# Optimization experiments

Measured on AMD Instinct MI355X. Metric: run time of the kernel, lower is better.

## Reference

```python
import jax, jax.numpy as jnp
import numpy as np

BN_EPS = 1e-5
SAMPLE_KEY = jax.random.key(42)


def setup_inputs() -> dict:
    key = jax.random.key(0)
    ks = jax.random.split(key, 12)
    B, W, E = 524288, 8, 4
    D = W * E  # 32, input dim of fc1

    def lin(k, fan_in, fan_out):
        k1, k2 = jax.random.split(k)
        bound = 1.0 / np.sqrt(fan_in)
        w = jax.random.uniform(k1, (fan_in, fan_out), jnp.float32, -bound, bound)
        b = jax.random.uniform(k2, (fan_out,), jnp.float32, -bound, bound)
        return w, b

    W1, b1 = lin(ks[0], D, 50)
    W2, b2 = lin(ks[1], 50, 30)
    W3, b3 = lin(ks[2], 30, 20)
    W4, b4 = lin(ks[3], 20, 15)
    W5, b5 = lin(ks[4], 15, W)
    # BatchNorm affine params (eval mode, running_mean=0, running_var=1)
    g1, be1 = jnp.ones((50,), jnp.float32), jnp.zeros((50,), jnp.float32)
    g2, be2 = jnp.ones((30,), jnp.float32), jnp.zeros((30,), jnp.float32)
    g3, be3 = jnp.ones((20,), jnp.float32), jnp.zeros((20,), jnp.float32)
    events = jax.random.normal(ks[5], (B, W, E), jnp.float32)
    return {"events": events,
            "W1": W1, "b1": b1, "g1": g1, "be1": be1,
            "W2": W2, "b2": b2, "g2": g2, "be2": be2,
            "W3": W3, "b3": b3, "g3": g3, "be3": be3,
            "W4": W4, "b4": b4, "W5": W5, "b5": b5}


def _bn_eval(x, g, b):
    # eval-mode BatchNorm1d with running_mean=0, running_var=1
    return x * (g / jnp.sqrt(1.0 + BN_EPS)) + b


def _probs(events, W1, b1, g1, be1, W2, b2, g2, be2, W3, b3, g3, be3, W4, b4, W5, b5):
    B = events.shape[0]
    x = events.reshape(B, -1)  # (B, window*event_size)
    h = jax.nn.relu(_bn_eval(x @ W1 + b1, g1, be1))
    h = jax.nn.relu(_bn_eval(h @ W2 + b2, g2, be2))
    h = jax.nn.relu(_bn_eval(h @ W3 + b3, g3, be3))
    h = jax.nn.relu(h @ W4 + b4)
    return jax.nn.sigmoid(h @ W5 + b5)  # (B, window_size)


def reference(events, W1, b1, g1, be1, W2, b2, g2, be2, W3, b3, g3, be3, W4, b4, W5, b5):
    p = _probs(events, W1, b1, g1, be1, W2, b2, g2, be2, W3, b3, g3, be3, W4, b4, W5, b5)
    # np.random.choice([0,1], p=[p, 1-p]) => P(choice=1) = 1 - p
    choice = jax.random.bernoulli(SAMPLE_KEY, 1.0 - p).astype(p.dtype)  # (B, W)
    chosen_events_np = 1.0 - choice
    flipped = jnp.abs(choice - p)            # prob of sampled outcome per element
    log_prob = jnp.log(jnp.prod(flipped, axis=1))  # (B,)
    return chosen_events_np, log_prob
```

## Files before the change

### kernel.cpp

```cpp
#include <hip/hip_runtime.h>
#include <math.h>

#define THREADS 256
#define TPW 4
#define ROWS_PER_BLOCK 256
#define P_MARGIN 2e-4f
#define FIXCAP 64

typedef float f32x4 __attribute__((ext_vector_type(4)));
typedef short short8 __attribute__((ext_vector_type(8)));
union Frag { unsigned u[4]; short8 s; };

#define FR1 0
#define FR2 2048
#define FR3 4096
#define VB1 5120
#define VS1 5170
#define VE1 5220
#define VB2 5270
#define VS2 5300
#define VE2 5330
#define VB3 5360
#define VS3 5380
#define VE3 5400
#define VB4 5420
#define VB5 5435
#define ACT 5460
#define WPOOL (ACT + 4 * 1088)
#define FRT4 ACT
#define FRT5 (ACT + 512)

__device__ __forceinline__ void tf2x32(unsigned x0, unsigned x1,
                                       unsigned &o0, unsigned &o1) {
  const unsigned k0 = 0u;
  const unsigned k1 = 42u;
  const unsigned k2 = 0x1BD11BDAu ^ k0 ^ k1;
  x0 += k0; x1 += k1;
#define TF_R(r) { x0 += x1; x1 = (x1 << (r)) | (x1 >> (32 - (r))); x1 ^= x0; }
  TF_R(13) TF_R(15) TF_R(26) TF_R(6)
  x0 += k1; x1 += k2 + 1u;
  TF_R(17) TF_R(29) TF_R(16) TF_R(24)
  x0 += k2; x1 += k0 + 2u;
  TF_R(13) TF_R(15) TF_R(26) TF_R(6)
  x0 += k0; x1 += k1 + 3u;
  TF_R(17) TF_R(29) TF_R(16) TF_R(24)
  x0 += k1; x1 += k2 + 4u;
  TF_R(13) TF_R(15) TF_R(26) TF_R(6)
  x0 += k2; x1 += k0 + 5u;
#undef TF_R
  o0 = x0; o1 = x1;
}

__device__ __forceinline__ unsigned rtnb(float v) {
  unsigned b = __float_as_uint(v);
  return (b + 0x7FFFu + ((b >> 16) & 1u)) & 0xFFFF0000u;
}

__device__ __forceinline__ unsigned cvtpk(float a, float b) {
  unsigned r;
  asm("v_cvt_pk_bf16_f32 %0, %1, %2" : "=v"(r) : "v"(a), "v"(b));
  return r;
}

__device__ __forceinline__ void pack8(const float f[8], short8 &H, short8 &L) {
  Frag h, l;
#pragma unroll
  for (int d = 0; d < 4; ++d) {
    unsigned hd = cvtpk(f[2 * d], f[2 * d + 1]);
    h.u[d] = hd;
    float r0 = f[2 * d]     - __uint_as_float(hd << 16);
    float r1 = f[2 * d + 1] - __uint_as_float(hd & 0xFFFF0000u);
    l.u[d] = cvtpk(r0, r1);
  }
  H = h.s; L = l.s;
}

__device__ __forceinline__ f32x4 mfma16(short8 a, short8 b, f32x4 c) {
  return __builtin_amdgcn_mfma_f32_16x16x32_bf16(a, b, c, 0, 0, 0);
}

__device__ __forceinline__ short8 ldfrag(const float *sW, int dwoff) {
  return *reinterpret_cast<const short8 *>(sW + dwoff);
}

template <int K, int N, int NT, int FB>
__device__ __forceinline__ void stage_layer(const float *__restrict__ W,
                                            float *sW, int t) {
  for (int i = t; i < K * N; i += THREADS) {
    int k = i / N, c = i - k * N;
    float v = W[i];
    unsigned hb = rtnb(v);
    float lov = v - __uint_as_float(hb);
    unsigned lb = rtnb(lov);
    int kt = k >> 5, gg = (k >> 3) & 3, d = (k >> 1) & 3, par = k & 1;
    int nt = c >> 4, lane = gg * 16 + (c & 15);
    int combo = kt * NT + nt;
    int dwhi = FB + (combo * 2 + 0) * 256 + lane * 4 + d;
    unsigned short *hp = reinterpret_cast<unsigned short *>(sW);
    hp[2 * dwhi + par] = (unsigned short)(hb >> 16);
    hp[2 * (dwhi + 256) + par] = (unsigned short)(lb >> 16);
  }
}

__device__ __forceinline__ void loadA(const float *actw, int kbase, int c,
                                      int g, short8 &H, short8 &L) {
  float f[8];
#pragma unroll
  for (int e = 0; e < 8; ++e) f[e] = actw[(kbase + g * 8 + e) * 17 + c];
  pack8(f, H, L);
}

__global__ __launch_bounds__(THREADS, 2)
void wtf_kernel(const float* __restrict__ events,
                const float* __restrict__ W1, const float* __restrict__ b1,
                const float* __restrict__ g1, const float* __restrict__ be1,
                const float* __restrict__ W2, const float* __restrict__ b2,
                const float* __restrict__ g2, const float* __restrict__ be2,
                const float* __restrict__ W3, const float* __restrict__ b3,
                const float* __restrict__ g3, const float* __restrict__ be3,
                const float* __restrict__ W4, const float* __restrict__ b4,
                const float* __restrict__ W5, const float* __restrict__ b5,
                float* __restrict__ out_chosen,
                float* __restrict__ out_logp,
                int B) {
  __shared__ float sW[WPOOL];
  __shared__ unsigned s_cnt;
  __shared__ unsigned s_rows[FIXCAP];

  const int t = threadIdx.x;
  const float rden = (float)(1.0 / sqrt(1.0 + 1e-5));

  if (t == 0) s_cnt = 0;
  for (int i = t; i < ACT + 1024; i += THREADS) sW[i] = 0.f;
  __syncthreads();
  stage_layer<32, 50, 4, FR1>(W1, sW, t);
  stage_layer<50, 30, 2, FR2>(W2, sW, t);
  stage_layer<30, 20, 2, FR3>(W3, sW, t);
  stage_layer<20, 15, 1, FRT4>(W4, sW, t);
  stage_layer<15, 8, 1, FRT5>(W5, sW, t);
  if (t < 50)                  { sW[VB1 + t] = b1[t]; sW[VS1 + t] = g1[t] * rden; sW[VE1 + t] = be1[t]; }
  else if (t >= 64 && t < 94)  { int i = t - 64;  sW[VB2 + i] = b2[i]; sW[VS2 + i] = g2[i] * rden; sW[VE2 + i] = be2[i]; }
  else if (t >= 128 && t < 148){ int i = t - 128; sW[VB3 + i] = b3[i]; sW[VS3 + i] = g3[i] * rden; sW[VE3 + i] = be3[i]; }
  else if (t >= 192 && t < 207){ sW[VB4 + (t - 192)] = b4[t - 192]; }
  else if (t >= 224 && t < 232){ sW[VB5 + (t - 224)] = b5[t - 224]; }
  __syncthreads();

  const int w = t >> 6, lane = t & 63;
  const int c = lane & 15, g = lane >> 4;

  const short8 bh4 = ldfrag(sW, FRT4 + lane * 4);
  const short8 bl4 = ldfrag(sW, FRT4 + 256 + lane * 4);
  const short8 bh5 = ldfrag(sW, FRT5 + lane * 4);
  const short8 bl5 = ldfrag(sW, FRT5 + 256 + lane * 4);
  __syncthreads();

  float *actw = sW + ACT + w * 1088;
  float *ptw  = actw + 544;

  const int wrow0 = blockIdx.x * ROWS_PER_BLOCK + w * (TPW * 16);
  const float4 *xp = reinterpret_cast<const float4 *>(
      events + (size_t)(wrow0 + c) * 32 + g * 8);
  float4 xa = xp[0], xb = xp[1];

#pragma unroll 1
  for (int tt = 0; tt < TPW; ++tt) {
    const int r0 = wrow0 + tt * 16;

    float xf[8] = {xa.x, xa.y, xa.z, xa.w, xb.x, xb.y, xb.z, xb.w};
    short8 Xh, Xl; pack8(xf, Xh, Xl);
    const int ttn = (tt + 1 < TPW) ? tt + 1 : tt;
    xa = xp[ttn * 128]; xb = xp[ttn * 128 + 1];

    {
      f32x4 acc[4];
#pragma unroll
      for (int nt = 0; nt < 4; ++nt) {
        float bb = sW[VB1 + nt * 16 + c];
        f32x4 ci = {bb, bb, bb, bb};
        short8 bh = ldfrag(sW, FR1 + (nt * 2 + 0) * 256 + lane * 4);
        short8 bl = ldfrag(sW, FR1 + (nt * 2 + 1) * 256 + lane * 4);
        ci = mfma16(Xl, bh, ci);
        ci = mfma16(Xh, bl, ci);
        acc[nt] = mfma16(Xh, bh, ci);
      }
#pragma unroll
      for (int nt = 0; nt < 4; ++nt) {
        float sc = sW[VS1 + nt * 16 + c], of = sW[VE1 + nt * 16 + c];
#pragma unroll
        for (int r = 0; r < 4; ++r)
          actw[(nt * 16 + c) * 17 + g * 4 + r] =
              fmaxf(fmaf(acc[nt][r], sc, of), 0.f);
      }
    }

    {
      f32x4 acc[2];
#pragma unroll
      for (int nt = 0; nt < 2; ++nt) {
        float bb = sW[VB2 + nt * 16 + c];
        acc[nt] = f32x4{bb, bb, bb, bb};
      }
#pragma unroll
      for (int kt = 0; kt < 2; ++kt) {
        short8 Ah, Al; loadA(actw, kt * 32, c, g, Ah, Al);
#pragma unroll
        for (int nt = 0; nt < 2; ++nt) {
          short8 bh = ldfrag(sW, FR2 + ((kt * 2 + nt) * 2 + 0) * 256 + lane * 4);
          short8 bl = ldfrag(sW, FR2 + ((kt * 2 + nt) * 2 + 1) * 256 + lane * 4);
          acc[nt] = mfma16(Al, bh, acc[nt]);
          acc[nt] = mfma16(Ah, bl, acc[nt]);
          acc[nt] = mfma16(Ah, bh, acc[nt]);
        }
      }
#pragma unroll
      for (int nt = 0; nt < 2; ++nt) {
        float sc = sW[VS2 + nt * 16 + c], of = sW[VE2 + nt * 16 + c];
#pragma unroll
        for (int r = 0; r < 4; ++r)
          actw[(nt * 16 + c) * 17 + g * 4 + r] =
              fmaxf(fmaf(acc[nt][r], sc, of), 0.f);
      }
    }

    {
      f32x4 acc[2];
#pragma unroll
      for (int nt = 0; nt < 2; ++nt) {
        float bb = sW[VB3 + nt * 16 + c];
        acc[nt] = f32x4{bb, bb, bb, bb};
      }
      short8 Ah, Al; loadA(actw, 0, c, g, Ah, Al);
#pragma unroll
      for (int nt = 0; nt < 2; ++nt) {
        short8 bh = ldfrag(sW, FR3 + (nt * 2 + 0) * 256 + lane * 4);
        short8 bl = ldfrag(sW, FR3 + (nt * 2 + 1) * 256 + lane * 4);
        acc[nt] = mfma16(Al, bh, acc[nt]);
        acc[nt] = mfma16(Ah, bl, acc[nt]);
        acc[nt] = mfma16(Ah, bh, acc[nt]);
      }
#pragma unroll
      for (int nt = 0; nt < 2; ++nt) {
        float sc = sW[VS3 + nt * 16 + c], of = sW[VE3 + nt * 16 + c];
#pragma unroll
        for (int r = 0; r < 4; ++r)
          actw[(nt * 16 + c) * 17 + g * 4 + r] =
              fmaxf(fmaf(acc[nt][r], sc, of), 0.f);
      }
    }

    {
      float bb = sW[VB4 + c];
      f32x4 acc = {bb, bb, bb, bb};
      short8 Ah, Al; loadA(actw, 0, c, g, Ah, Al);
      acc = mfma16(Al, bh4, acc);
      acc = mfma16(Ah, bl4, acc);
      acc = mfma16(Ah, bh4, acc);
#pragma unroll
      for (int r = 0; r < 4; ++r) {
        actw[c * 17 + g * 4 + r] = fmaxf(acc[r], 0.f);
        actw[(16 + c) * 17 + g * 4 + r] = 0.f;
      }
    }

    {
      float bb = sW[VB5 + c];
      f32x4 acc = {bb, bb, bb, bb};
      short8 Ah, Al; loadA(actw, 0, c, g, Ah, Al);
      acc = mfma16(Al, bh5, acc);
      acc = mfma16(Ah, bl5, acc);
      acc = mfma16(Ah, bh5, acc);
      if (c < 8) {
#pragma unroll
        for (int r = 0; r < 4; ++r) ptw[(g * 4 + r) * 9 + c] = acc[r];
      }
    }

    {
      const int erow = lane >> 2, cp = lane & 3;
      const int grow = r0 + erow;
      float l0 = ptw[erow * 9 + 2 * cp];
      float l1 = ptw[erow * 9 + 2 * cp + 1];
      float p0 = 1.f / (1.f + __expf(-l0));
      float p1 = 1.f / (1.f + __expf(-l1));
      unsigned o0, o1, q0, q1;
      tf2x32(0u, 8u * (unsigned)grow + 2u * cp,      o0, o1);
      tf2x32(0u, 8u * (unsigned)grow + 2u * cp + 1u, q0, q1);
      float u0 = __uint_as_float(0x3F800000u | ((o0 ^ o1) >> 9)) - 1.f;
      float u1 = __uint_as_float(0x3F800000u | ((q0 ^ q1) >> 9)) - 1.f;
      float th0 = 1.f - p0, th1 = 1.f - p1;
      bool c0 = u0 < th0, c1 = u1 < th1;
      bool need = (fabsf(u0 - th0) < P_MARGIN) || (fabsf(u1 - th1) < P_MARGIN);
      float prod = (c0 ? th0 : p0) * (c1 ? th1 : p1);
      prod *= __shfl_xor(prod, 1);
      prod *= __shfl_xor(prod, 2);
      float2 chv = make_float2(c0 ? 0.f : 1.f, c1 ? 0.f : 1.f);
      *reinterpret_cast<float2 *>(out_chosen + (size_t)grow * 8 + 2 * cp) = chv;
      if (cp == 0) out_logp[grow] = __logf(prod);
      if (need) {
        unsigned i = atomicAdd(&s_cnt, 1u);
        if (i < FIXCAP) s_rows[i] = (unsigned)grow;
      }
    }
  }

  __syncthreads();
  unsigned cnt = s_cnt;
  if (cnt > FIXCAP) cnt = FIXCAP;
  if (cnt == 0) return;

  double *sA = reinterpret_cast<double *>(sW + ACT);
  double *sB = sA + 64;
  double *sF = sB + 64;

  const double denom = sqrt(1.0 + 1e-5);
  for (unsigned r = 0; r < cnt; ++r) {
    const int rb = (int)s_rows[r];

    if (t < 32) sA[t] = (double)events[(size_t)rb * 32 + t];
    __syncthreads();

    double v = 0.0;
    if (t < 50) {
#pragma unroll
      for (int k = 0; k < 32; ++k) v = fma(sA[k], (double)W1[k * 50 + t], v);
      v += (double)b1[t];
      v = v * ((double)g1[t] / denom) + (double)be1[t];
      v = v > 0.0 ? v : 0.0;
    }
    __syncthreads();
    if (t < 50) sB[t] = v;
    __syncthreads();

    v = 0.0;
    if (t < 30) {
#pragma unroll
      for (int k = 0; k < 50; ++k) v = fma(sB[k], (double)W2[k * 30 + t], v);
      v += (double)b2[t];
      v = v * ((double)g2[t] / denom) + (double)be2[t];
      v = v > 0.0 ? v : 0.0;
    }
    __syncthreads();
    if (t < 30) sA[t] = v;
    __syncthreads();

    v = 0.0;
    if (t < 20) {
#pragma unroll
      for (int k = 0; k < 30; ++k) v = fma(sA[k], (double)W3[k * 20 + t], v);
      v += (double)b3[t];
      v = v * ((double)g3[t] / denom) + (double)be3[t];
      v = v > 0.0 ? v : 0.0;
    }
    __syncthreads();
    if (t < 20) sB[t] = v;
    __syncthreads();

    v = 0.0;
    if (t < 15) {
#pragma unroll
      for (int k = 0; k < 20; ++k) v = fma(sB[k], (double)W4[k * 15 + t], v);
      v += (double)b4[t];
      v = v > 0.0 ? v : 0.0;
    }
    __syncthreads();
    if (t < 15) sA[t] = v;
    __syncthreads();

    if (t < 8) {
      v = 0.0;
#pragma unroll
      for (int k = 0; k < 15; ++k) v = fma(sA[k], (double)W5[k * 8 + t], v);
      v += (double)b5[t];
      double p = 1.0 / (1.0 + exp(-v));
      unsigned j = 8u * (unsigned)rb + (unsigned)t, o0, o1;
      tf2x32(0u, j, o0, o1);
      unsigned bits = o0 ^ o1;
      float u = __uint_as_float(0x3F800000u | (bits >> 9)) - 1.f;
      double thr = 1.0 - p;
      bool choice = ((double)u < thr);
      out_chosen[(size_t)rb * 8 + t] = choice ? 0.f : 1.f;
      sF[t] = choice ? thr : p;
    }
    __syncthreads();
    if (t == 0) {
      double prod = 1.0;
      for (int w2 = 0; w2 < 8; ++w2) prod *= sF[w2];
      out_logp[rb] = (float)log(prod);
    }
    __syncthreads();
  }
}

extern "C" void kernel_launch(void* const* d_in, const int* in_sizes, int n_in,
                              void* d_out, int out_size, void* d_ws, size_t ws_size,
                              hipStream_t stream) {
  const float* events = (const float*)d_in[0];
  const float* W1  = (const float*)d_in[1];
  const float* b1  = (const float*)d_in[2];
  const float* g1  = (const float*)d_in[3];
  const float* be1 = (const float*)d_in[4];
  const float* W2  = (const float*)d_in[5];
  const float* b2  = (const float*)d_in[6];
  const float* g2  = (const float*)d_in[7];
  const float* be2 = (const float*)d_in[8];
  const float* W3  = (const float*)d_in[9];
  const float* b3  = (const float*)d_in[10];
  const float* g3  = (const float*)d_in[11];
  const float* be3 = (const float*)d_in[12];
  const float* W4  = (const float*)d_in[13];
  const float* b4  = (const float*)d_in[14];
  const float* W5  = (const float*)d_in[15];
  const float* b5  = (const float*)d_in[16];

  const int B = in_sizes[0] / 32;
  float* out = (float*)d_out;
  float* out_chosen = out;
  float* out_logp   = out + (size_t)B * 8;

  const int blocks = (B + ROWS_PER_BLOCK - 1) / ROWS_PER_BLOCK;
  hipLaunchKernelGGL(wtf_kernel, dim3(blocks), dim3(THREADS), 0, stream,
                     events, W1, b1, g1, be1, W2, b2, g2, be2,
                     W3, b3, g3, be3, W4, b4, W5, b5,
                     out_chosen, out_logp, B);
}
```

Baseline: 223.8 us.

## Keep MLP activations in registers by transposing MFMA operands and permuting weight tiles

```diff
diff --git a/kernel.cpp b/kernel.cpp
--- a/kernel.cpp
+++ b/kernel.cpp
@@ -14,21 +14,21 @@
 #define FR1 0
 #define FR2 2048
 #define FR3 4096
-#define VB1 5120
-#define VS1 5170
-#define VE1 5220
-#define VB2 5270
-#define VS2 5300
-#define VE2 5330
-#define VB3 5360
-#define VS3 5380
-#define VE3 5400
-#define VB4 5420
-#define VB5 5435
-#define ACT 5460
-#define WPOOL (ACT + 4 * 1088)
-#define FRT4 ACT
-#define FRT5 (ACT + 512)
+#define FR4 5120
+#define FR5 6144
+#define VB1 6656
+#define VS1 6708
+#define VE1 6760
+#define VB2 6812
+#define VS2 6844
+#define VE2 6876
+#define VB3 6908
+#define VS3 6928
+#define VE3 6948
+#define VB4 6968
+#define VB5 6984
+#define PZ  6992
+#define WPOOL 7024
 
 __device__ __forceinline__ void tf2x32(unsigned x0, unsigned x1,
                                        unsigned &o0, unsigned &o1) {
@@ -82,31 +82,46 @@
 __device__ __forceinline__ short8 ldfrag(const float *sW, int dwoff) {
   return *reinterpret_cast<const short8 *>(sW + dwoff);
 }
-
-template <int K, int N, int NT, int FB>
-__device__ __forceinline__ void stage_layer(const float *__restrict__ W,
-                                            float *sW, int t) {
+__device__ __forceinline__ f32x4 ldv4(const float *sW, int dwoff) {
+  return *reinterpret_cast<const f32x4 *>(sW + dwoff);
+}
+
+template <int K, int N, int NT, int FB, bool PERM>
+__device__ __forceinline__ void stageA(const float *__restrict__ W,
+                                       float *sW, int t) {
   for (int i = t; i < K * N; i += THREADS) {
-    int k = i / N, c = i - k * N;
+    int k = i / N, n = i - k * N;
     float v = W[i];
     unsigned hb = rtnb(v);
-    float lov = v - __uint_as_float(hb);
-    unsigned lb = rtnb(lov);
-    int kt = k >> 5, gg = (k >> 3) & 3, d = (k >> 1) & 3, par = k & 1;
-    int nt = c >> 4, lane = gg * 16 + (c & 15);
-    int combo = kt * NT + nt;
-    int dwhi = FB + (combo * 2 + 0) * 256 + lane * 4 + d;
+    unsigned lb = rtnb(v - __uint_as_float(hb));
+    int kt = k >> 5, g = (k >> 3) & 3, e = k & 7, d = e >> 1, par = e & 1;
+    int tile, r;
+    if (PERM) {
+      int pg = n >> 5, m = n & 31, tt = (m >> 2) & 1;
+      r = ((m >> 3) << 2) | (m & 3);
+      tile = pg * 2 + tt;
+    } else {
+      tile = n >> 4; r = n & 15;
+    }
+    int lane = g * 16 + r;
+    int dwhi = FB + (kt * NT + tile) * 512 + lane * 4 + d;
     unsigned short *hp = reinterpret_cast<unsigned short *>(sW);
     hp[2 * dwhi + par] = (unsigned short)(hb >> 16);
     hp[2 * (dwhi + 256) + par] = (unsigned short)(lb >> 16);
   }
 }
 
-__device__ __forceinline__ void loadA(const float *actw, int kbase, int c,
-                                      int g, short8 &H, short8 &L) {
+__device__ __forceinline__ void bnpack(f32x4 a0, f32x4 a1, const float *sW,
+                                       int vs, int ve, int g,
+                                       short8 &H, short8 &L) {
+  f32x4 sc0 = ldv4(sW, vs + g * 8),     of0 = ldv4(sW, ve + g * 8);
+  f32x4 sc1 = ldv4(sW, vs + g * 8 + 4), of1 = ldv4(sW, ve + g * 8 + 4);
   float f[8];
 #pragma unroll
-  for (int e = 0; e < 8; ++e) f[e] = actw[(kbase + g * 8 + e) * 17 + c];
+  for (int q = 0; q < 4; ++q) {
+    f[q]     = fmaxf(fmaf(a0[q], sc0[q], of0[q]), 0.f);
+    f[4 + q] = fmaxf(fmaf(a1[q], sc1[q], of1[q]), 0.f);
+  }
   pack8(f, H, L);
 }
 
@@ -126,18 +141,21 @@
   __shared__ float sW[WPOOL];
   __shared__ unsigned s_cnt;
   __shared__ unsigned s_rows[FIXCAP];
+  __shared__ double sA[64];
+  __shared__ double sB[64];
+  __shared__ double sF[8];
 
   const int t = threadIdx.x;
   const float rden = (float)(1.0 / sqrt(1.0 + 1e-5));
 
   if (t == 0) s_cnt = 0;
-  for (int i = t; i < ACT + 1024; i += THREADS) sW[i] = 0.f;
+  for (int i = t; i < WPOOL; i += THREADS) sW[i] = 0.f;
   __syncthreads();
-  stage_layer<32, 50, 4, FR1>(W1, sW, t);
-  stage_layer<50, 30, 2, FR2>(W2, sW, t);
-  stage_layer<30, 20, 2, FR3>(W3, sW, t);
-  stage_layer<20, 15, 1, FRT4>(W4, sW, t);
-  stage_layer<15, 8, 1, FRT5>(W5, sW, t);
+  stageA<32, 50, 4, FR1, true>(W1, sW, t);
+  stageA<50, 30, 2, FR2, true>(W2, sW, t);
+  stageA<30, 20, 2, FR3, true>(W3, sW, t);
+  stageA<20, 15, 2, FR4, true>(W4, sW, t);
+  stageA<15,  8, 1, FR5, false>(W5, sW, t);
   if (t < 50)                  { sW[VB1 + t] = b1[t]; sW[VS1 + t] = g1[t] * rden; sW[VE1 + t] = be1[t]; }
   else if (t >= 64 && t < 94)  { int i = t - 64;  sW[VB2 + i] = b2[i]; sW[VS2 + i] = g2[i] * rden; sW[VE2 + i] = be2[i]; }
   else if (t >= 128 && t < 148){ int i = t - 128; sW[VB3 + i] = b3[i]; sW[VS3 + i] = g3[i] * rden; sW[VE3 + i] = be3[i]; }
@@ -147,15 +165,7 @@
 
   const int w = t >> 6, lane = t & 63;
   const int c = lane & 15, g = lane >> 4;
-
-  const short8 bh4 = ldfrag(sW, FRT4 + lane * 4);
-  const short8 bl4 = ldfrag(sW, FRT4 + 256 + lane * 4);
-  const short8 bh5 = ldfrag(sW, FRT5 + lane * 4);
-  const short8 bl5 = ldfrag(sW, FRT5 + 256 + lane * 4);
-  __syncthreads();
-
-  float *actw = sW + ACT + w * 1088;
-  float *ptw  = actw + 544;
+  const int labase = lane * 4;
 
   const int wrow0 = blockIdx.x * ROWS_PER_BLOCK + w * (TPW * 16);
   const float4 *xp = reinterpret_cast<const float4 *>(
@@ -165,140 +175,117 @@
 #pragma unroll 1
   for (int tt = 0; tt < TPW; ++tt) {
     const int r0 = wrow0 + tt * 16;
+    const int row = r0 + c;
 
     float xf[8] = {xa.x, xa.y, xa.z, xa.w, xb.x, xb.y, xb.z, xb.w};
     short8 Xh, Xl; pack8(xf, Xh, Xl);
     const int ttn = (tt + 1 < TPW) ? tt + 1 : tt;
     xa = xp[ttn * 128]; xb = xp[ttn * 128 + 1];
 
+    f32x4 a1[4];
+#pragma unroll
+    for (int ti = 0; ti < 4; ++ti) {
+      f32x4 acc = ldv4(sW, VB1 + (ti >> 1) * 32 + g * 8 + (ti & 1) * 4);
+      short8 wh = ldfrag(sW, FR1 + ti * 512 + labase);
+      short8 wl = ldfrag(sW, FR1 + ti * 512 + 256 + labase);
+      acc = mfma16(wh, Xl, acc);
+      acc = mfma16(wl, Xh, acc);
+      a1[ti] = mfma16(wh, Xh, acc);
+    }
+
+    short8 B2h[2], B2l[2];
+    bnpack(a1[0], a1[1], sW, VS1,      VE1,      g, B2h[0], B2l[0]);
+    bnpack(a1[2], a1[3], sW, VS1 + 32, VE1 + 32, g, B2h[1], B2l[1]);
+
+    f32x4 a2[2];
+#pragma unroll
+    for (int ti = 0; ti < 2; ++ti) {
+      f32x4 acc = ldv4(sW, VB2 + g * 8 + ti * 4);
+#pragma unroll
+      for (int kt = 0; kt < 2; ++kt) {
+        short8 wh = ldfrag(sW, FR2 + (kt * 2 + ti) * 512 + labase);
+        short8 wl = ldfrag(sW, FR2 + (kt * 2 + ti) * 512 + 256 + labase);
+        acc = mfma16(wh, B2l[kt], acc);
+        acc = mfma16(wl, B2h[kt], acc);
+        acc = mfma16(wh, B2h[kt], acc);
+      }
+      a2[ti] = acc;
+    }
+
+    short8 B3h, B3l;
+    bnpack(a2[0], a2[1], sW, VS2, VE2, g, B3h, B3l);
+
+    f32x4 a3[2];
+#pragma unroll
+    for (int ti = 0; ti < 2; ++ti) {
+      f32x4 acc = ldv4(sW, VB3 + g * 8 + ti * 4);
+      short8 wh = ldfrag(sW, FR3 + ti * 512 + labase);
+      short8 wl = ldfrag(sW, FR3 + ti * 512 + 256 + labase);
+      acc = mfma16(wh, B3l, acc);
+      acc = mfma16(wl, B3h, acc);
+      a3[ti] = mfma16(wh, B3h, acc);
+    }
+
+    short8 B4h, B4l;
+    bnpack(a3[0], a3[1], sW, VS3, VE3, g, B4h, B4l);
+
+    f32x4 a4[2];
+#pragma unroll
+    for (int ti = 0; ti < 2; ++ti) {
+      f32x4 acc = ldv4(sW, VB4 + g * 8 + ti * 4);
+      short8 wh = ldfrag(sW, FR4 + ti * 512 + labase);
+      short8 wl = ldfrag(sW, FR4 + ti * 512 + 256 + labase);
+      acc = mfma16(wh, B4l, acc);
+      acc = mfma16(wl, B4h, acc);
+      a4[ti] = mfma16(wh, B4h, acc);
+    }
+
+    short8 B5h, B5l;
     {
-      f32x4 acc[4];
-#pragma unroll
-      for (int nt = 0; nt < 4; ++nt) {
-        float bb = sW[VB1 + nt * 16 + c];
-        f32x4 ci = {bb, bb, bb, bb};
-        short8 bh = ldfrag(sW, FR1 + (nt * 2 + 0) * 256 + lane * 4);
-        short8 bl = ldfrag(sW, FR1 + (nt * 2 + 1) * 256 + lane * 4);
-        ci = mfma16(Xl, bh, ci);
-        ci = mfma16(Xh, bl, ci);
-        acc[nt] = mfma16(Xh, bh, ci);
+      float f[8];
+#pragma unroll
+      for (int q = 0; q < 4; ++q) {
+        f[q]     = fmaxf(a4[0][q], 0.f);
+        f[4 + q] = fmaxf(a4[1][q], 0.f);
       }
-#pragma unroll
-      for (int nt = 0; nt < 4; ++nt) {
-        float sc = sW[VS1 + nt * 16 + c], of = sW[VE1 + nt * 16 + c];
-#pragma unroll
-        for (int r = 0; r < 4; ++r)
-          actw[(nt * 16 + c) * 17 + g * 4 + r] =
-              fmaxf(fmaf(acc[nt][r], sc, of), 0.f);
-      }
-    }
-
+      pack8(f, B5h, B5l);
+    }
+
+    f32x4 a5;
     {
-      f32x4 acc[2];
-#pragma unroll
-      for (int nt = 0; nt < 2; ++nt) {
-        float bb = sW[VB2 + nt * 16 + c];
-        acc[nt] = f32x4{bb, bb, bb, bb};
-      }
-#pragma unroll
-      for (int kt = 0; kt < 2; ++kt) {
-        short8 Ah, Al; loadA(actw, kt * 32, c, g, Ah, Al);
-#pragma unroll
-        for (int nt = 0; nt < 2; ++nt) {
-          short8 bh = ldfrag(sW, FR2 + ((kt * 2 + nt) * 2 + 0) * 256 + lane * 4);
-          short8 bl = ldfrag(sW, FR2 + ((kt * 2 + nt) * 2 + 1) * 256 + lane * 4);
-          acc[nt] = mfma16(Al, bh, acc[nt]);
-          acc[nt] = mfma16(Ah, bl, acc[nt]);
-          acc[nt] = mfma16(Ah, bh, acc[nt]);
-        }
-      }
-#pragma unroll
-      for (int nt = 0; nt < 2; ++nt) {
-        float sc = sW[VS2 + nt * 16 + c], of = sW[VE2 + nt * 16 + c];
-#pragma unroll
-        for (int r = 0; r < 4; ++r)
-          actw[(nt * 16 + c) * 17 + g * 4 + r] =
-              fmaxf(fmaf(acc[nt][r], sc, of), 0.f);
-      }
+      f32x4 acc = ldv4(sW, VB5 + g * 4);
+      short8 wh = ldfrag(sW, FR5 + labase);
+      short8 wl = ldfrag(sW, FR5 + 256 + labase);
+      acc = mfma16(wh, B5l, acc);
+      acc = mfma16(wl, B5h, acc);
+      a5 = mfma16(wh, B5h, acc);
     }
 
     {
-      f32x4 acc[2];
-#pragma unroll
-      for (int nt = 0; nt < 2; ++nt) {
-        float bb = sW[VB3 + nt * 16 + c];
-        acc[nt] = f32x4{bb, bb, bb, bb};
-      }
-      short8 Ah, Al; loadA(actw, 0, c, g, Ah, Al);
-#pragma unroll
-      for (int nt = 0; nt < 2; ++nt) {
-        short8 bh = ldfrag(sW, FR3 + (nt * 2 + 0) * 256 + lane * 4);
-        short8 bl = ldfrag(sW, FR3 + (nt * 2 + 1) * 256 + lane * 4);
-        acc[nt] = mfma16(Al, bh, acc[nt]);
-        acc[nt] = mfma16(Ah, bl, acc[nt]);
-        acc[nt] = mfma16(Ah, bh, acc[nt]);
-      }
-#pragma unroll
-      for (int nt = 0; nt < 2; ++nt) {
-        float sc = sW[VS3 + nt * 16 + c], of = sW[VE3 + nt * 16 + c];
-#pragma unroll
-        for (int r = 0; r < 4; ++r)
-          actw[(nt * 16 + c) * 17 + g * 4 + r] =
-              fmaxf(fmaf(acc[nt][r], sc, of), 0.f);
-      }
-    }
-
-    {
-      float bb = sW[VB4 + c];
-      f32x4 acc = {bb, bb, bb, bb};
-      short8 Ah, Al; loadA(actw, 0, c, g, Ah, Al);
-      acc = mfma16(Al, bh4, acc);
-      acc = mfma16(Ah, bl4, acc);
-      acc = mfma16(Ah, bh4, acc);
-#pragma unroll
-      for (int r = 0; r < 4; ++r) {
-        actw[c * 17 + g * 4 + r] = fmaxf(acc[r], 0.f);
-        actw[(16 + c) * 17 + g * 4 + r] = 0.f;
-      }
-    }
-
-    {
-      float bb = sW[VB5 + c];
-      f32x4 acc = {bb, bb, bb, bb};
-      short8 Ah, Al; loadA(actw, 0, c, g, Ah, Al);
-      acc = mfma16(Al, bh5, acc);
-      acc = mfma16(Ah, bl5, acc);
-      acc = mfma16(Ah, bh5, acc);
-      if (c < 8) {
-#pragma unroll
-        for (int r = 0; r < 4; ++r) ptw[(g * 4 + r) * 9 + c] = acc[r];
-      }
-    }
-
-    {
-      const int erow = lane >> 2, cp = lane & 3;
-      const int grow = r0 + erow;
-      float l0 = ptw[erow * 9 + 2 * cp];
-      float l1 = ptw[erow * 9 + 2 * cp + 1];
+      float s2v = __shfl_xor(a5[2], 32);
+      float s3v = __shfl_xor(a5[3], 32);
+      float l0 = (g < 2) ? a5[0] : s2v;
+      float l1 = (g < 2) ? a5[1] : s3v;
+      const int base = ((g & 1) << 2) | ((g >> 1) << 1);
       float p0 = 1.f / (1.f + __expf(-l0));
       float p1 = 1.f / (1.f + __expf(-l1));
       unsigned o0, o1, q0, q1;
-      tf2x32(0u, 8u * (unsigned)grow + 2u * cp,      o0, o1);
-      tf2x32(0u, 8u * (unsigned)grow + 2u * cp + 1u, q0, q1);
+      tf2x32(0u, 8u * (unsigned)row + (unsigned)base,      o0, o1);
+      tf2x32(0u, 8u * (unsigned)row + (unsigned)base + 1u, q0, q1);
       float u0 = __uint_as_float(0x3F800000u | ((o0 ^ o1) >> 9)) - 1.f;
       float u1 = __uint_as_float(0x3F800000u | ((q0 ^ q1) >> 9)) - 1.f;
       float th0 = 1.f - p0, th1 = 1.f - p1;
       bool c0 = u0 < th0, c1 = u1 < th1;
       bool need = (fabsf(u0 - th0) < P_MARGIN) || (fabsf(u1 - th1) < P_MARGIN);
       float prod = (c0 ? th0 : p0) * (c1 ? th1 : p1);
-      prod *= __shfl_xor(prod, 1);
-      prod *= __shfl_xor(prod, 2);
+      prod *= __shfl_xor(prod, 16);
+      prod *= __shfl_xor(prod, 32);
       float2 chv = make_float2(c0 ? 0.f : 1.f, c1 ? 0.f : 1.f);
-      *reinterpret_cast<float2 *>(out_chosen + (size_t)grow * 8 + 2 * cp) = chv;
-      if (cp == 0) out_logp[grow] = __logf(prod);
+      *reinterpret_cast<float2 *>(out_chosen + (size_t)row * 8 + base) = chv;
+      if (g == 0) out_logp[row] = __logf(prod);
       if (need) {
         unsigned i = atomicAdd(&s_cnt, 1u);
-        if (i < FIXCAP) s_rows[i] = (unsigned)grow;
+        if (i < FIXCAP) s_rows[i] = (unsigned)row;
       }
     }
   }
@@ -307,10 +294,6 @@
   unsigned cnt = s_cnt;
   if (cnt > FIXCAP) cnt = FIXCAP;
   if (cnt == 0) return;
-
-  double *sA = reinterpret_cast<double *>(sW + ACT);
-  double *sB = sA + 64;
-  double *sF = sB + 64;
 
   const double denom = sqrt(1.0 + 1e-5);
   for (unsigned r = 0; r < cnt; ++r) {
```

Result: no change. 222.9 us (-0.4%).
